# Kernel optimization log

Measured on AMD Instinct MI355X. Metric: run time of the kernel, lower is better.

Reference implementation:

```python
import jax, jax.numpy as jnp
import numpy as np

N = 50000      # nodes
E = 800000     # edges (before self loops)
NFEAT = 128
HEADS = 4
NCLASS = 32    # per-head out channels of each GATConv
NHID = HEADS * NCLASS  # 128, inter-layer width
NEG_SLOPE = 0.2


def setup_inputs() -> dict:
    key = jax.random.key(0)
    ks = jax.random.split(key, 10)
    x = jax.random.normal(ks[0], (N, NFEAT), dtype=jnp.float32)
    adj = jax.random.randint(ks[1], (2, E), 0, N, dtype=jnp.int32)

    def glorot(k, shape):
        fan = shape[0] + shape[-1]
        return jax.random.normal(k, shape, dtype=jnp.float32) * jnp.sqrt(2.0 / fan)

    # conv1: nfeat -> heads*nclass
    W1 = glorot(ks[2], (NFEAT, HEADS * NCLASS))
    att_src1 = glorot(ks[3], (HEADS, NCLASS))
    att_dst1 = glorot(ks[4], (HEADS, NCLASS))
    b1 = jnp.zeros((HEADS * NCLASS,), dtype=jnp.float32)
    # conv2: nhid -> heads*nclass
    W2 = glorot(ks[5], (NHID, HEADS * NCLASS))
    att_src2 = glorot(ks[6], (HEADS, NCLASS))
    att_dst2 = glorot(ks[7], (HEADS, NCLASS))
    b2 = jnp.zeros((HEADS * NCLASS,), dtype=jnp.float32)
    return {"x": x, "adj": adj,
            "W1": W1, "att_src1": att_src1, "att_dst1": att_dst1, "b1": b1,
            "W2": W2, "att_src2": att_src2, "att_dst2": att_dst2, "b2": b2}


def gat_conv(x, src, dst, n, W, att_src, att_dst, bias):
    """PyG GATConv (concat=True, inference): gather -> edge attention -> segment softmax -> scatter."""
    H, C = att_src.shape
    h = (x @ W).reshape(n, H, C)                    # [N,H,C]
    a_s = jnp.sum(h * att_src[None], axis=-1)       # [N,H]
    a_d = jnp.sum(h * att_dst[None], axis=-1)       # [N,H]
    e = jax.nn.leaky_relu(a_s[src] + a_d[dst], NEG_SLOPE)  # [E,H]
    # numerically-stable segment softmax over edges grouped by destination node
    m = jax.ops.segment_max(e, dst, num_segments=n)        # [N,H]
    m = jnp.where(jnp.isfinite(m), m, 0.0)
    ex = jnp.exp(e - m[dst])                               # [E,H]
    denom = jax.ops.segment_sum(ex, dst, num_segments=n)   # [N,H]
    alpha = ex / (denom[dst] + 1e-16)                      # [E,H]
    out = jax.ops.segment_sum(h[src] * alpha[:, :, None], dst, num_segments=n)  # [N,H,C]
    return out.reshape(n, H * C) + bias


def reference(x, adj, W1, att_src1, att_dst1, b1, W2, att_src2, att_dst2, b2):
    # PyG GATConv adds self loops by default
    loops = jnp.arange(N, dtype=adj.dtype)
    src = jnp.concatenate([adj[0], loops])
    dst = jnp.concatenate([adj[1], loops])
    h = jax.nn.relu(gat_conv(x, src, dst, N, W1, att_src1, att_dst1, b1))
    # dropout is identity in eval mode
    out = gat_conv(h, src, dst, N, W2, att_src2, att_dst2, b2)
    return out
```

## Files before the change

### kernel.cpp

```cpp
#include <hip/hip_runtime.h>
#include <hip/hip_fp16.h>

#define N_NODES 50000
#define E_EDGES 800000
#define ETOT    (E_EDGES + N_NODES)
#define NF      128
#define HEADS   4
#define NC      32
#define LOG2E   1.44269504088896340736f
#define ASTRIDE 136
#define CAP     96

#define NBUCK   196
#define EPB     4096
#define NBLKA   ((ETOT + EPB - 1) / EPB)
#define PARTN   (NBUCK * NBLKA)
#define NBLKS   ((PARTN + 255) / 256)
#define WCB     65

typedef __attribute__((ext_vector_type(8))) short short8v;
typedef __attribute__((ext_vector_type(4))) float f32x4;

__device__ inline ushort rne_bf16(float x) {
    uint u = __float_as_uint(x);
    return (ushort)((u + 0x7fff + ((u >> 16) & 1)) >> 16);
}
__device__ inline float h2f_lo(uint u) { return __half2float(__ushort_as_half((ushort)(u & 0xffffu))); }
__device__ inline float h2f_hi(uint u) { return __half2float(__ushort_as_half((ushort)(u >> 16))); }

__device__ inline void wconv_body(int wb, int tid, const float* __restrict__ W,
                                  const float* __restrict__ att_src,
                                  const float* __restrict__ att_dst,
                                  ushort* __restrict__ Wt) {
    if (wb < 64) {
        int i = wb * 256 + tid;
        int k = i >> 7, n = i & 127;
        Wt[n * 144 + k] = rne_bf16(W[i]);
    } else {
        for (int j = tid; j < 1024; j += 256) {
            int k = j >> 3, o = j & 7;
            int h = o & 3;
            const float* av = (o < 4) ? att_src : att_dst;
            float s = 0.f;
            #pragma unroll
            for (int c = 0; c < 32; ++c) s += W[k * 128 + h * 32 + c] * av[h * 32 + c];
            Wt[(128 + o) * 144 + k] = rne_bf16(s * LOG2E);
        }
        for (int j = tid; j < 8 * 144; j += 256)
            Wt[(136 + (j / 144)) * 144 + (j % 144)] = 0;
    }
}

__global__ __launch_bounds__(256) void prep_kernel(const int* __restrict__ adj,
                                                   int* __restrict__ partials,
                                                   const float* __restrict__ W1,
                                                   const float* __restrict__ as1,
                                                   const float* __restrict__ ad1,
                                                   ushort* __restrict__ Wt1,
                                                   const float* __restrict__ W2,
                                                   const float* __restrict__ as2,
                                                   const float* __restrict__ ad2,
                                                   ushort* __restrict__ Wt2) {
    __shared__ int lc[NBUCK];
    int b = blockIdx.x, tid = threadIdx.x;
    if (b < NBLKA) {
        for (int i = tid; i < NBUCK; i += 256) lc[i] = 0;
        __syncthreads();
        int base = b * EPB;
        #pragma unroll
        for (int i = 0; i < EPB / 256; ++i) {
            int e = base + i * 256 + tid;
            if (e < ETOT) {
                int dst = (e < E_EDGES) ? adj[E_EDGES + e] : (e - E_EDGES);
                atomicAdd(&lc[dst >> 8], 1);
            }
        }
        __syncthreads();
        for (int i = tid; i < NBUCK; i += 256) partials[i * NBLKA + b] = lc[i];
    } else {
        int wb = b - NBLKA;
        if (wb < WCB) wconv_body(wb, tid, W1, as1, ad1, Wt1);
        else          wconv_body(wb - WCB, tid, W2, as2, ad2, Wt2);
    }
}

__device__ inline int block_incl_scan(int v, int* sh4) {
    int lane = threadIdx.x & 63, wid = threadIdx.x >> 6;
    int s = v;
    #pragma unroll
    for (int ofs = 1; ofs < 64; ofs <<= 1) {
        int t = __shfl_up(s, ofs);
        if (lane >= ofs) s += t;
    }
    if (lane == 63) sh4[wid] = s;
    __syncthreads();
    int add = 0;
    #pragma unroll
    for (int k = 0; k < 3; ++k) if (k < wid) add += sh4[k];
    return s + add;
}

__global__ __launch_bounds__(256) void bsum2_kernel(const int* __restrict__ partials,
                                                    int* __restrict__ bsum) {
    __shared__ int sh4[4];
    int i = blockIdx.x * 256 + threadIdx.x;
    int v = (i < PARTN) ? partials[i] : 0;
    int s = block_incl_scan(v, sh4);
    if (threadIdx.x == 255) bsum[blockIdx.x] = s;
}

__global__ __launch_bounds__(256) void scan_bsums2_kernel(const int* __restrict__ bsum,
                                                          int* __restrict__ bofs) {
    __shared__ int sh4[4];
    int i = threadIdx.x;
    int v = (i < NBLKS) ? bsum[i] : 0;
    int s = block_incl_scan(v, sh4);
    if (i < NBLKS) bofs[i] = s - v;
}

__global__ __launch_bounds__(256) void scan_final2_kernel(const int* __restrict__ partials,
                                                          const int* __restrict__ bofs,
                                                          int* __restrict__ pscan) {
    __shared__ int sh4[4];
    int i = blockIdx.x * 256 + threadIdx.x;
    int v = (i < PARTN) ? partials[i] : 0;
    int s = block_incl_scan(v, sh4);
    if (i < PARTN) pscan[i] = bofs[blockIdx.x] + s - v;
}

__global__ __launch_bounds__(256) void pass_scatter_kernel(const int* __restrict__ adj,
                                                           const int* __restrict__ pscan,
                                                           int2* __restrict__ ebuf) {
    __shared__ int lc[NBUCK];
    int tid = threadIdx.x;
    for (int i = tid; i < NBUCK; i += 256) lc[i] = 0;
    __syncthreads();
    int base = blockIdx.x * EPB;
    #pragma unroll
    for (int i = 0; i < EPB / 256; ++i) {
        int e = base + i * 256 + tid;
        if (e < ETOT) {
            int src, dst;
            if (e < E_EDGES) { src = adj[e]; dst = adj[E_EDGES + e]; }
            else             { src = dst = e - E_EDGES; }
            int b = dst >> 8;
            int r = atomicAdd(&lc[b], 1);
            ebuf[pscan[b * NBLKA + blockIdx.x] + r] = make_int2(src, dst);
        }
    }
}

__global__ __launch_bounds__(256) void pass_build_kernel(const int2* __restrict__ ebuf,
                                                         const int* __restrict__ pscan,
                                                         int* __restrict__ cnt,
                                                         int* __restrict__ slots) {
    __shared__ int lc[256];
    int tid = threadIdx.x;
    int b = blockIdx.x;
    lc[tid] = 0;
    __syncthreads();
    int base = pscan[b * NBLKA];
    int end  = (b == NBUCK - 1) ? ETOT : pscan[(b + 1) * NBLKA];
    for (int e = base + tid; e < end; e += 256) {
        int2 sd = ebuf[e];
        int d = sd.y & 255;
        int r = atomicAdd(&lc[d], 1);
        slots[(size_t)sd.y * CAP + r] = sd.x;
    }
    __syncthreads();
    int dst = b * 256 + tid;
    if (dst < N_NODES) cnt[dst] = lc[tid];
}

template<bool BF16IN>
__global__ __launch_bounds__(256) void gemm_mfma_kernel(const void* __restrict__ Xv_,
                                                        const ushort* __restrict__ Wt,
                                                        ushort* __restrict__ Hf,
                                                        float* __restrict__ a_s,
                                                        float* __restrict__ a_d, int nrows) {
    __shared__ ushort Abf[64 * ASTRIDE];
    int tid = threadIdx.x;
    int r0 = blockIdx.x * 64;
    int rleft = nrows - r0;

    if (BF16IN) {
        const uint4* Xv = (const uint4*)((const ushort*)Xv_ + (size_t)r0 * NF);
        #pragma unroll
        for (int p = 0; p < 4; ++p) {
            int i = p * 256 + tid;
            int row = i >> 4, c8 = i & 15;
            uint4 v = (row < rleft) ? Xv[row * 16 + c8] : make_uint4(0u, 0u, 0u, 0u);
            *(uint4*)&Abf[row * ASTRIDE + c8 * 8] = v;
        }
    } else {
        const float4* Xv = (const float4*)((const float*)Xv_ + (size_t)r0 * NF);
        #pragma unroll
        for (int p = 0; p < 8; ++p) {
            int i = p * 256 + tid;
            int row = i >> 5, c4 = i & 31;
            float4 v = (row < rleft) ? Xv[row * 32 + c4] : make_float4(0.f, 0.f, 0.f, 0.f);
            ushort4 hv;
            hv.x = rne_bf16(v.x); hv.y = rne_bf16(v.y);
            hv.z = rne_bf16(v.z); hv.w = rne_bf16(v.w);
            *(ushort4*)&Abf[row * ASTRIDE + c4 * 4] = hv;
        }
    }
    __syncthreads();

    int wv = tid >> 6;
    int l = tid & 63;
    int lr = l & 15;
    int lk = l >> 4;
    int rowb = wv * 16;

    short8v a[4];
    #pragma unroll
    for (int kc = 0; kc < 4; ++kc)
        a[kc] = *(const short8v*)&Abf[(rowb + lr) * ASTRIDE + kc * 32 + lk * 8];

    f32x4 acc[9];
    #pragma unroll
    for (int ct = 0; ct < 9; ++ct) acc[ct] = (f32x4){0.f, 0.f, 0.f, 0.f};

    #pragma unroll
    for (int ct = 0; ct < 9; ++ct) {
        #pragma unroll
        for (int kc = 0; kc < 4; ++kc) {
            short8v b = *(const short8v*)&Wt[(ct * 16 + lr) * 144 + kc * 32 + lk * 8];
            acc[ct] = __builtin_amdgcn_mfma_f32_16x16x32_bf16(a[kc], b, acc[ct], 0, 0, 0);
        }
    }

    int rbase = r0 + rowb + lk * 4;
    #pragma unroll
    for (int ct = 0; ct < 8; ++ct) {
        int col = ct * 16 + lr;
        #pragma unroll
        for (int ri = 0; ri < 4; ++ri) {
            int r = rbase + ri;
            if (r < nrows) Hf[(size_t)r * NF + col] = __half_as_ushort(__float2half(acc[ct][ri]));
        }
    }
    if (lr < 8) {
        #pragma unroll
        for (int ri = 0; ri < 4; ++ri) {
            int r = rbase + ri;
            if (r < nrows) {
                if (lr < 4) a_s[(size_t)r * 4 + lr] = acc[8][ri];
                else        a_d[(size_t)r * 4 + (lr - 4)] = acc[8][ri];
            }
        }
    }
}

template<int WRITE_BF16>
__global__ __launch_bounds__(256) void agg_kernel(const ushort* __restrict__ Hf,
                                                  const float* __restrict__ a_s,
                                                  const float* __restrict__ a_d,
                                                  const int* __restrict__ cnt,
                                                  const int* __restrict__ slots,
                                                  const float* __restrict__ bias,
                                                  void* __restrict__ Out) {
    int lane = threadIdx.x & 63;
    int node = blockIdx.x * 4 + (threadIdx.x >> 6);
    if (node >= N_NODES) return;
    int q = lane >> 4;
    int t = lane & 15;
    int h = t >> 2;
    float adn = a_d[node * 4 + h];
    int deg = cnt[node];
    const int* row = slots + (size_t)node * CAP;
    const uint4* H4 = (const uint4*)Hf;
    float acc[8];
    #pragma unroll
    for (int k = 0; k < 8; ++k) acc[k] = 0.f;
    float denom = 0.f;

    for (int j = 0; j < deg; j += 8) {
        int sv[2]; float ev[2]; uint4 hv[2]; bool ok[2];
        #pragma unroll
        for (int u = 0; u < 2; ++u) {
            int idx = j + u * 4 + q;
            ok[u] = idx < deg;
            sv[u] = row[ok[u] ? idx : 0];
        }
        #pragma unroll
        for (int u = 0; u < 2; ++u) ev[u] = a_s[sv[u] * 4 + h];
        #pragma unroll
        for (int u = 0; u < 2; ++u) hv[u] = H4[(size_t)sv[u] * 16 + t];
        #pragma unroll
        for (int u = 0; u < 2; ++u) {
            float e = ev[u] + adn;
            e = (e > 0.f) ? e : 0.2f * e;
            float w = ok[u] ? exp2f(e) : 0.f;
            denom += w;
            acc[0] = fmaf(h2f_lo(hv[u].x), w, acc[0]);
            acc[1] = fmaf(h2f_hi(hv[u].x), w, acc[1]);
            acc[2] = fmaf(h2f_lo(hv[u].y), w, acc[2]);
            acc[3] = fmaf(h2f_hi(hv[u].y), w, acc[3]);
            acc[4] = fmaf(h2f_lo(hv[u].z), w, acc[4]);
            acc[5] = fmaf(h2f_hi(hv[u].z), w, acc[5]);
            acc[6] = fmaf(h2f_lo(hv[u].w), w, acc[6]);
            acc[7] = fmaf(h2f_hi(hv[u].w), w, acc[7]);
        }
    }
    #pragma unroll
    for (int ofs = 16; ofs < 64; ofs <<= 1) {
        denom += __shfl_xor(denom, ofs);
        #pragma unroll
        for (int k = 0; k < 8; ++k) acc[k] += __shfl_xor(acc[k], ofs);
    }
    if (q == 0) {
        float inv = 1.f / (denom + 1e-16f);
        float4 b0 = ((const float4*)bias)[t * 2];
        float4 b1 = ((const float4*)bias)[t * 2 + 1];
        float v0 = acc[0] * inv + b0.x, v1 = acc[1] * inv + b0.y;
        float v2 = acc[2] * inv + b0.z, v3 = acc[3] * inv + b0.w;
        float v4 = acc[4] * inv + b1.x, v5 = acc[5] * inv + b1.y;
        float v6 = acc[6] * inv + b1.z, v7 = acc[7] * inv + b1.w;
        if (WRITE_BF16) {
            v0 = fmaxf(v0, 0.f); v1 = fmaxf(v1, 0.f); v2 = fmaxf(v2, 0.f); v3 = fmaxf(v3, 0.f);
            v4 = fmaxf(v4, 0.f); v5 = fmaxf(v5, 0.f); v6 = fmaxf(v6, 0.f); v7 = fmaxf(v7, 0.f);
            uint4 pv;
            pv.x = (uint)rne_bf16(v0) | ((uint)rne_bf16(v1) << 16);
            pv.y = (uint)rne_bf16(v2) | ((uint)rne_bf16(v3) << 16);
            pv.z = (uint)rne_bf16(v4) | ((uint)rne_bf16(v5) << 16);
            pv.w = (uint)rne_bf16(v6) | ((uint)rne_bf16(v7) << 16);
            ((uint4*)((ushort*)Out + (size_t)node * NF))[t] = pv;
        } else {
            float4* orow = (float4*)((float*)Out + (size_t)node * NF);
            orow[t * 2]     = make_float4(v0, v1, v2, v3);
            orow[t * 2 + 1] = make_float4(v4, v5, v6, v7);
        }
    }
}

extern "C" void kernel_launch(void* const* d_in, const int* in_sizes, int n_in,
                              void* d_out, int out_size, void* d_ws, size_t ws_size,
                              hipStream_t stream) {
    const float* x        = (const float*)d_in[0];
    const int*   adj      = (const int*)  d_in[1];
    const float* W1       = (const float*)d_in[2];
    const float* att_src1 = (const float*)d_in[3];
    const float* att_dst1 = (const float*)d_in[4];
    const float* b1       = (const float*)d_in[5];
    const float* W2       = (const float*)d_in[6];
    const float* att_src2 = (const float*)d_in[7];
    const float* att_dst2 = (const float*)d_in[8];
    const float* b2       = (const float*)d_in[9];
    float* out = (float*)d_out;

    float* a_s  = (float*)d_ws;
    float* a_d  = a_s + (size_t)N_NODES * HEADS;
    ushort* Hf  = (ushort*)(a_d + (size_t)N_NODES * HEADS);
    ushort* obf = Hf + (size_t)N_NODES * NF;
    ushort* Wt1 = obf + (size_t)N_NODES * NF;
    ushort* Wt2 = Wt1 + 144 * 144;
    int* cnt     = (int*)(Wt2 + 144 * 144);
    int* slots   = cnt + N_NODES;
    int* partials= slots + (size_t)N_NODES * CAP;
    int* pscan   = partials + PARTN;
    int* bsum    = pscan + PARTN;
    int* bofs    = bsum + NBLKS;
    int2* ebuf   = (int2*)(bofs + NBLKS + 2);

    prep_kernel<<<NBLKA + 2 * WCB, 256, 0, stream>>>(adj, partials,
                                                     W1, att_src1, att_dst1, Wt1,
                                                     W2, att_src2, att_dst2, Wt2);
    bsum2_kernel<<<NBLKS, 256, 0, stream>>>(partials, bsum);
    scan_bsums2_kernel<<<1, 256, 0, stream>>>(bsum, bofs);
    scan_final2_kernel<<<NBLKS, 256, 0, stream>>>(partials, bofs, pscan);
    pass_scatter_kernel<<<NBLKA, 256, 0, stream>>>(adj, pscan, ebuf);
    pass_build_kernel<<<NBUCK, 256, 0, stream>>>(ebuf, pscan, cnt, slots);

    gemm_mfma_kernel<false><<<(N_NODES + 63) / 64, 256, 0, stream>>>(x, Wt1, Hf, a_s, a_d, N_NODES);
    agg_kernel<1><<<(N_NODES + 3) / 4, 256, 0, stream>>>(Hf, a_s, a_d, cnt, slots, b1, obf);

    gemm_mfma_kernel<true><<<(N_NODES + 63) / 64, 256, 0, stream>>>(obf, Wt2, Hf, a_s, a_d, N_NODES);
    agg_kernel<0><<<(N_NODES + 3) / 4, 256, 0, stream>>>(Hf, a_s, a_d, cnt, slots, b2, out);
}
```

Before: 149.3 us.

## Fuse CSR build pipeline into one cooperative kernel with grid syncs

Merges the six preprocessing kernels (bucket count plus weight conversion, three scan stages, scatter and slot build) into one cooperative launch that separates phases with grid-wide barriers. The aim is to remove five kernel launch gaps and their inter-kernel idle time. In exchange, every phase runs with the same grid size, roughly 338 blocks, so most blocks sit idle in the small scan phases. It also depends on all blocks being co-resident and on the cost of each grid.sync.

Measured after the change: 352.0 us. 136% more time.

```diff
diff --git a/kernel.cpp b/kernel.cpp
--- a/kernel.cpp
+++ b/kernel.cpp
@@ -1,5 +1,8 @@
 #include <hip/hip_runtime.h>
 #include <hip/hip_fp16.h>
+#include <hip/hip_cooperative_groups.h>
+
+namespace cg = cooperative_groups;
 
 #define N_NODES 50000
 #define E_EDGES 800000
@@ -17,6 +20,7 @@
 #define PARTN   (NBUCK * NBLKA)
 #define NBLKS   ((PARTN + 255) / 256)
 #define WCB     65
+#define COOPB   (NBLKA + 2 * WCB)
 
 typedef __attribute__((ext_vector_type(8))) short short8v;
 typedef __attribute__((ext_vector_type(4))) float f32x4;
@@ -51,18 +55,43 @@
     }
 }
 
-__global__ __launch_bounds__(256) void prep_kernel(const int* __restrict__ adj,
-                                                   int* __restrict__ partials,
-                                                   const float* __restrict__ W1,
-                                                   const float* __restrict__ as1,
-                                                   const float* __restrict__ ad1,
-                                                   ushort* __restrict__ Wt1,
-                                                   const float* __restrict__ W2,
-                                                   const float* __restrict__ as2,
-                                                   const float* __restrict__ ad2,
-                                                   ushort* __restrict__ Wt2) {
-    __shared__ int lc[NBUCK];
+__device__ inline int block_incl_scan(int v, int* sh4) {
+    int lane = threadIdx.x & 63, wid = threadIdx.x >> 6;
+    int s = v;
+    #pragma unroll
+    for (int ofs = 1; ofs < 64; ofs <<= 1) {
+        int t = __shfl_up(s, ofs);
+        if (lane >= ofs) s += t;
+    }
+    if (lane == 63) sh4[wid] = s;
+    __syncthreads();
+    int add = 0;
+    #pragma unroll
+    for (int k = 0; k < 3; ++k) if (k < wid) add += sh4[k];
+    return s + add;
+}
+
+__global__ __launch_bounds__(256) void csr_coop_kernel(const int* __restrict__ adj,
+                                                       int* __restrict__ partials,
+                                                       const float* __restrict__ W1,
+                                                       const float* __restrict__ as1,
+                                                       const float* __restrict__ ad1,
+                                                       ushort* __restrict__ Wt1,
+                                                       const float* __restrict__ W2,
+                                                       const float* __restrict__ as2,
+                                                       const float* __restrict__ ad2,
+                                                       ushort* __restrict__ Wt2,
+                                                       int* __restrict__ bsum,
+                                                       int* __restrict__ bofs,
+                                                       int* __restrict__ pscan,
+                                                       int2* __restrict__ ebuf,
+                                                       int* __restrict__ cnt,
+                                                       int* __restrict__ slots) {
+    cg::grid_group grid = cg::this_grid();
+    __shared__ int lc[256];
+    __shared__ int sh4[4];
     int b = blockIdx.x, tid = threadIdx.x;
+
     if (b < NBLKA) {
         for (int i = tid; i < NBUCK; i += 256) lc[i] = 0;
         __syncthreads();
@@ -82,94 +111,65 @@
         if (wb < WCB) wconv_body(wb, tid, W1, as1, ad1, Wt1);
         else          wconv_body(wb - WCB, tid, W2, as2, ad2, Wt2);
     }
-}
-
-__device__ inline int block_incl_scan(int v, int* sh4) {
-    int lane = threadIdx.x & 63, wid = threadIdx.x >> 6;
-    int s = v;
-    #pragma unroll
-    for (int ofs = 1; ofs < 64; ofs <<= 1) {
-        int t = __shfl_up(s, ofs);
-        if (lane >= ofs) s += t;
-    }
-    if (lane == 63) sh4[wid] = s;
-    __syncthreads();
-    int add = 0;
-    #pragma unroll
-    for (int k = 0; k < 3; ++k) if (k < wid) add += sh4[k];
-    return s + add;
-}
-
-__global__ __launch_bounds__(256) void bsum2_kernel(const int* __restrict__ partials,
-                                                    int* __restrict__ bsum) {
-    __shared__ int sh4[4];
-    int i = blockIdx.x * 256 + threadIdx.x;
-    int v = (i < PARTN) ? partials[i] : 0;
-    int s = block_incl_scan(v, sh4);
-    if (threadIdx.x == 255) bsum[blockIdx.x] = s;
-}
-
-__global__ __launch_bounds__(256) void scan_bsums2_kernel(const int* __restrict__ bsum,
-                                                          int* __restrict__ bofs) {
-    __shared__ int sh4[4];
-    int i = threadIdx.x;
-    int v = (i < NBLKS) ? bsum[i] : 0;
-    int s = block_incl_scan(v, sh4);
-    if (i < NBLKS) bofs[i] = s - v;
-}
-
-__global__ __launch_bounds__(256) void scan_final2_kernel(const int* __restrict__ partials,
-                                                          const int* __restrict__ bofs,
-                                                          int* __restrict__ pscan) {
-    __shared__ int sh4[4];
-    int i = blockIdx.x * 256 + threadIdx.x;
-    int v = (i < PARTN) ? partials[i] : 0;
-    int s = block_incl_scan(v, sh4);
-    if (i < PARTN) pscan[i] = bofs[blockIdx.x] + s - v;
-}
-
-__global__ __launch_bounds__(256) void pass_scatter_kernel(const int* __restrict__ adj,
-                                                           const int* __restrict__ pscan,
-                                                           int2* __restrict__ ebuf) {
-    __shared__ int lc[NBUCK];
-    int tid = threadIdx.x;
-    for (int i = tid; i < NBUCK; i += 256) lc[i] = 0;
-    __syncthreads();
-    int base = blockIdx.x * EPB;
-    #pragma unroll
-    for (int i = 0; i < EPB / 256; ++i) {
-        int e = base + i * 256 + tid;
-        if (e < ETOT) {
-            int src, dst;
-            if (e < E_EDGES) { src = adj[e]; dst = adj[E_EDGES + e]; }
-            else             { src = dst = e - E_EDGES; }
-            int b = dst >> 8;
-            int r = atomicAdd(&lc[b], 1);
-            ebuf[pscan[b * NBLKA + blockIdx.x] + r] = make_int2(src, dst);
-        }
-    }
-}
-
-__global__ __launch_bounds__(256) void pass_build_kernel(const int2* __restrict__ ebuf,
-                                                         const int* __restrict__ pscan,
-                                                         int* __restrict__ cnt,
-                                                         int* __restrict__ slots) {
-    __shared__ int lc[256];
-    int tid = threadIdx.x;
-    int b = blockIdx.x;
-    lc[tid] = 0;
-    __syncthreads();
-    int base = pscan[b * NBLKA];
-    int end  = (b == NBUCK - 1) ? ETOT : pscan[(b + 1) * NBLKA];
-    for (int e = base + tid; e < end; e += 256) {
-        int2 sd = ebuf[e];
-        int d = sd.y & 255;
-        int r = atomicAdd(&lc[d], 1);
-        slots[(size_t)sd.y * CAP + r] = sd.x;
-    }
-    __syncthreads();
-    int dst = b * 256 + tid;
-    if (dst < N_NODES) cnt[dst] = lc[tid];
+    grid.sync();
+
+    if (b < NBLKS) {
+        int i = b * 256 + tid;
+        int v = (i < PARTN) ? partials[i] : 0;
+        int s = block_incl_scan(v, sh4);
+        if (tid == 255) bsum[b] = s;
+    }
+    grid.sync();
+
+    if (b == 0) {
+        int v = (tid < NBLKS) ? bsum[tid] : 0;
+        int s = block_incl_scan(v, sh4);
+        if (tid < NBLKS) bofs[tid] = s - v;
+    }
+    grid.sync();
+
+    if (b < NBLKS) {
+        int i = b * 256 + tid;
+        int v = (i < PARTN) ? partials[i] : 0;
+        int s = block_incl_scan(v, sh4);
+        if (i < PARTN) pscan[i] = bofs[b] + s - v;
+    }
+    grid.sync();
+
+    if (b < NBLKA) {
+        for (int i = tid; i < NBUCK; i += 256) lc[i] = 0;
+        __syncthreads();
+        int base = b * EPB;
+        #pragma unroll
+        for (int i = 0; i < EPB / 256; ++i) {
+            int e = base + i * 256 + tid;
+            if (e < ETOT) {
+                int src, dst;
+                if (e < E_EDGES) { src = adj[e]; dst = adj[E_EDGES + e]; }
+                else             { src = dst = e - E_EDGES; }
+                int bk = dst >> 8;
+                int r = atomicAdd(&lc[bk], 1);
+                ebuf[pscan[bk * NBLKA + b] + r] = make_int2(src, dst);
+            }
+        }
+    }
+    grid.sync();
+
+    if (b < NBUCK) {
+        lc[tid] = 0;
+        __syncthreads();
+        int base = pscan[b * NBLKA];
+        int end  = (b == NBUCK - 1) ? ETOT : pscan[(b + 1) * NBLKA];
+        for (int e = base + tid; e < end; e += 256) {
+            int2 sd = ebuf[e];
+            int d = sd.y & 255;
+            int r = atomicAdd(&lc[d], 1);
+            slots[(size_t)sd.y * CAP + r] = sd.x;
+        }
+        __syncthreads();
+        int dst = b * 256 + tid;
+        if (dst < N_NODES) cnt[dst] = lc[tid];
+    }
 }
 
 template<bool BF16IN>
@@ -364,14 +364,15 @@
     int* bofs    = bsum + NBLKS;
     int2* ebuf   = (int2*)(bofs + NBLKS + 2);
 
-    prep_kernel<<<NBLKA + 2 * WCB, 256, 0, stream>>>(adj, partials,
-                                                     W1, att_src1, att_dst1, Wt1,
-                                                     W2, att_src2, att_dst2, Wt2);
-    bsum2_kernel<<<NBLKS, 256, 0, stream>>>(partials, bsum);
-    scan_bsums2_kernel<<<1, 256, 0, stream>>>(bsum, bofs);
-    scan_final2_kernel<<<NBLKS, 256, 0, stream>>>(partials, bofs, pscan);
-    pass_scatter_kernel<<<NBLKA, 256, 0, stream>>>(adj, pscan, ebuf);
-    pass_build_kernel<<<NBUCK, 256, 0, stream>>>(ebuf, pscan, cnt, slots);
+    {
+        void* args[] = {(void*)&adj, (void*)&partials,
+                        (void*)&W1, (void*)&att_src1, (void*)&att_dst1, (void*)&Wt1,
+                        (void*)&W2, (void*)&att_src2, (void*)&att_dst2, (void*)&Wt2,
+                        (void*)&bsum, (void*)&bofs, (void*)&pscan,
+                        (void*)&ebuf, (void*)&cnt, (void*)&slots};
+        hipLaunchCooperativeKernel((const void*)csr_coop_kernel, dim3(COOPB), dim3(256),
+                                   args, 0, stream);
+    }
 
     gemm_mfma_kernel<false><<<(N_NODES + 63) / 64, 256, 0, stream>>>(x, Wt1, Hf, a_s, a_d, N_NODES);
     agg_kernel<1><<<(N_NODES + 3) / 4, 256, 0, stream>>>(Hf, a_s, a_d, cnt, slots, b1, obf);
```

## Merge block-sum scan into final scan and co-launch edge scatter with layer-1 GEMM

Applied to the files above, without the earlier changes.

Removes the single-block scan_bsums kernel: each scan_final block now recomputes its own prefix offset from the block sums. The edge-scatter pass and the layer-1 GEMM, which do not depend on each other, are merged into one heterogeneous kernel whose blocks branch on blockIdx, so both run concurrently. This cuts two launches and their serialization gaps. In exchange each scan block does redundant work, and the merged kernel has to size its shared memory for the larger of the two roles.

Result: faster. 140.5 us, median of 2 (-5.8%).

```diff
diff --git a/kernel.cpp b/kernel.cpp
--- a/kernel.cpp
+++ b/kernel.cpp
@@ -109,45 +109,137 @@
     if (threadIdx.x == 255) bsum[blockIdx.x] = s;
 }
 
-__global__ __launch_bounds__(256) void scan_bsums2_kernel(const int* __restrict__ bsum,
-                                                          int* __restrict__ bofs) {
-    __shared__ int sh4[4];
-    int i = threadIdx.x;
-    int v = (i < NBLKS) ? bsum[i] : 0;
-    int s = block_incl_scan(v, sh4);
-    if (i < NBLKS) bofs[i] = s - v;
-}
-
 __global__ __launch_bounds__(256) void scan_final2_kernel(const int* __restrict__ partials,
-                                                          const int* __restrict__ bofs,
+                                                          const int* __restrict__ bsum,
                                                           int* __restrict__ pscan) {
     __shared__ int sh4[4];
-    int i = blockIdx.x * 256 + threadIdx.x;
+    __shared__ int bofs_sh;
+    int b = blockIdx.x, tid = threadIdx.x;
+    int pv = (tid < NBLKS && tid < b) ? bsum[tid] : 0;
+    int ps = block_incl_scan(pv, sh4);
+    if (tid == 255) bofs_sh = ps;
+    __syncthreads();
+    int i = b * 256 + tid;
     int v = (i < PARTN) ? partials[i] : 0;
     int s = block_incl_scan(v, sh4);
-    if (i < PARTN) pscan[i] = bofs[blockIdx.x] + s - v;
-}
-
-__global__ __launch_bounds__(256) void pass_scatter_kernel(const int* __restrict__ adj,
-                                                           const int* __restrict__ pscan,
-                                                           int2* __restrict__ ebuf) {
-    __shared__ int lc[NBUCK];
-    int tid = threadIdx.x;
-    for (int i = tid; i < NBUCK; i += 256) lc[i] = 0;
-    __syncthreads();
-    int base = blockIdx.x * EPB;
-    #pragma unroll
-    for (int i = 0; i < EPB / 256; ++i) {
-        int e = base + i * 256 + tid;
-        if (e < ETOT) {
-            int src, dst;
-            if (e < E_EDGES) { src = adj[e]; dst = adj[E_EDGES + e]; }
-            else             { src = dst = e - E_EDGES; }
-            int b = dst >> 8;
-            int r = atomicAdd(&lc[b], 1);
-            ebuf[pscan[b * NBLKA + blockIdx.x] + r] = make_int2(src, dst);
-        }
-    }
+    if (i < PARTN) pscan[i] = bofs_sh + s - v;
+}
+
+template<bool BF16IN>
+__device__ inline void gemm_body(ushort* __restrict__ Abf, int tid, int r0,
+                                 const void* __restrict__ Xv_, const ushort* __restrict__ Wt,
+                                 ushort* __restrict__ Hf, float* __restrict__ a_s,
+                                 float* __restrict__ a_d, int nrows) {
+    int rleft = nrows - r0;
+    if (BF16IN) {
+        const uint4* Xv = (const uint4*)((const ushort*)Xv_ + (size_t)r0 * NF);
+        #pragma unroll
+        for (int p = 0; p < 4; ++p) {
+            int i = p * 256 + tid;
+            int row = i >> 4, c8 = i & 15;
+            uint4 v = (row < rleft) ? Xv[row * 16 + c8] : make_uint4(0u, 0u, 0u, 0u);
+            *(uint4*)&Abf[row * ASTRIDE + c8 * 8] = v;
+        }
+    } else {
+        const float4* Xv = (const float4*)((const float*)Xv_ + (size_t)r0 * NF);
+        #pragma unroll
+        for (int p = 0; p < 8; ++p) {
+            int i = p * 256 + tid;
+            int row = i >> 5, c4 = i & 31;
+            float4 v = (row < rleft) ? Xv[row * 32 + c4] : make_float4(0.f, 0.f, 0.f, 0.f);
+            ushort4 hv;
+            hv.x = rne_bf16(v.x); hv.y = rne_bf16(v.y);
+            hv.z = rne_bf16(v.z); hv.w = rne_bf16(v.w);
+            *(ushort4*)&Abf[row * ASTRIDE + c4 * 4] = hv;
+        }
+    }
+    __syncthreads();
+
+    int wv = tid >> 6;
+    int l = tid & 63;
+    int lr = l & 15;
+    int lk = l >> 4;
+    int rowb = wv * 16;
+
+    short8v a[4];
+    #pragma unroll
+    for (int kc = 0; kc < 4; ++kc)
+        a[kc] = *(const short8v*)&Abf[(rowb + lr) * ASTRIDE + kc * 32 + lk * 8];
+
+    f32x4 acc[9];
+    #pragma unroll
+    for (int ct = 0; ct < 9; ++ct) acc[ct] = (f32x4){0.f, 0.f, 0.f, 0.f};
+
+    #pragma unroll
+    for (int ct = 0; ct < 9; ++ct) {
+        #pragma unroll
+        for (int kc = 0; kc < 4; ++kc) {
+            short8v b = *(const short8v*)&Wt[(ct * 16 + lr) * 144 + kc * 32 + lk * 8];
+            acc[ct] = __builtin_amdgcn_mfma_f32_16x16x32_bf16(a[kc], b, acc[ct], 0, 0, 0);
+        }
+    }
+
+    int rbase = r0 + rowb + lk * 4;
+    #pragma unroll
+    for (int ct = 0; ct < 8; ++ct) {
+        int col = ct * 16 + lr;
+        #pragma unroll
+        for (int ri = 0; ri < 4; ++ri) {
+            int r = rbase + ri;
+            if (r < nrows) Hf[(size_t)r * NF + col] = __half_as_ushort(__float2half(acc[ct][ri]));
+        }
+    }
+    if (lr < 8) {
+        #pragma unroll
+        for (int ri = 0; ri < 4; ++ri) {
+            int r = rbase + ri;
+            if (r < nrows) {
+                if (lr < 4) a_s[(size_t)r * 4 + lr] = acc[8][ri];
+                else        a_d[(size_t)r * 4 + (lr - 4)] = acc[8][ri];
+            }
+        }
+    }
+}
+
+__global__ __launch_bounds__(256) void mid_kernel(const int* __restrict__ adj,
+                                                  const int* __restrict__ pscan,
+                                                  int2* __restrict__ ebuf,
+                                                  const float* __restrict__ X,
+                                                  const ushort* __restrict__ Wt,
+                                                  ushort* __restrict__ Hf,
+                                                  float* __restrict__ a_s,
+                                                  float* __restrict__ a_d, int nrows) {
+    __shared__ ushort Abf[64 * ASTRIDE];
+    int b = blockIdx.x, tid = threadIdx.x;
+    if (b < NBLKA) {
+        int* lc = (int*)Abf;
+        for (int i = tid; i < NBUCK; i += 256) lc[i] = 0;
+        __syncthreads();
+        int base = b * EPB;
+        #pragma unroll
+        for (int i = 0; i < EPB / 256; ++i) {
+            int e = base + i * 256 + tid;
+            if (e < ETOT) {
+                int src, dst;
+                if (e < E_EDGES) { src = adj[e]; dst = adj[E_EDGES + e]; }
+                else             { src = dst = e - E_EDGES; }
+                int bk = dst >> 8;
+                int r = atomicAdd(&lc[bk], 1);
+                ebuf[pscan[bk * NBLKA + b] + r] = make_int2(src, dst);
+            }
+        }
+    } else {
+        gemm_body<false>(Abf, tid, (b - NBLKA) * 64, X, Wt, Hf, a_s, a_d, nrows);
+    }
+}
+
+__global__ __launch_bounds__(256) void gemm_mfma_kernel(const void* __restrict__ Xv_,
+                                                        const ushort* __restrict__ Wt,
+                                                        ushort* __restrict__ Hf,
+                                                        float* __restrict__ a_s,
+                                                        float* __restrict__ a_d, int nrows) {
+    __shared__ ushort Abf[64 * ASTRIDE];
+    gemm_body<true>(Abf, threadIdx.x, blockIdx.x * 64, Xv_, Wt, Hf, a_s, a_d, nrows);
 }
 
 __global__ __launch_bounds__(256) void pass_build_kernel(const int2* __restrict__ ebuf,
@@ -170,87 +262,6 @@
     __syncthreads();
     int dst = b * 256 + tid;
     if (dst < N_NODES) cnt[dst] = lc[tid];
-}
-
-template<bool BF16IN>
-__global__ __launch_bounds__(256) void gemm_mfma_kernel(const void* __restrict__ Xv_,
-                                                        const ushort* __restrict__ Wt,
-                                                        ushort* __restrict__ Hf,
-                                                        float* __restrict__ a_s,
-                                                        float* __restrict__ a_d, int nrows) {
-    __shared__ ushort Abf[64 * ASTRIDE];
-    int tid = threadIdx.x;
-    int r0 = blockIdx.x * 64;
-    int rleft = nrows - r0;
-
-    if (BF16IN) {
-        const uint4* Xv = (const uint4*)((const ushort*)Xv_ + (size_t)r0 * NF);
-        #pragma unroll
-        for (int p = 0; p < 4; ++p) {
-            int i = p * 256 + tid;
-            int row = i >> 4, c8 = i & 15;
-            uint4 v = (row < rleft) ? Xv[row * 16 + c8] : make_uint4(0u, 0u, 0u, 0u);
-            *(uint4*)&Abf[row * ASTRIDE + c8 * 8] = v;
-        }
-    } else {
-        const float4* Xv = (const float4*)((const float*)Xv_ + (size_t)r0 * NF);
-        #pragma unroll
-        for (int p = 0; p < 8; ++p) {
-            int i = p * 256 + tid;
-            int row = i >> 5, c4 = i & 31;
-            float4 v = (row < rleft) ? Xv[row * 32 + c4] : make_float4(0.f, 0.f, 0.f, 0.f);
-            ushort4 hv;
-            hv.x = rne_bf16(v.x); hv.y = rne_bf16(v.y);
-            hv.z = rne_bf16(v.z); hv.w = rne_bf16(v.w);
-            *(ushort4*)&Abf[row * ASTRIDE + c4 * 4] = hv;
-        }
-    }
-    __syncthreads();
-
-    int wv = tid >> 6;
-    int l = tid & 63;
-    int lr = l & 15;
-    int lk = l >> 4;
-    int rowb = wv * 16;
-
-    short8v a[4];
-    #pragma unroll
-    for (int kc = 0; kc < 4; ++kc)
-        a[kc] = *(const short8v*)&Abf[(rowb + lr) * ASTRIDE + kc * 32 + lk * 8];
-
-    f32x4 acc[9];
-    #pragma unroll
-    for (int ct = 0; ct < 9; ++ct) acc[ct] = (f32x4){0.f, 0.f, 0.f, 0.f};
-
-    #pragma unroll
-    for (int ct = 0; ct < 9; ++ct) {
-        #pragma unroll
-        for (int kc = 0; kc < 4; ++kc) {
-            short8v b = *(const short8v*)&Wt[(ct * 16 + lr) * 144 + kc * 32 + lk * 8];
-            acc[ct] = __builtin_amdgcn_mfma_f32_16x16x32_bf16(a[kc], b, acc[ct], 0, 0, 0);
-        }
-    }
-
-    int rbase = r0 + rowb + lk * 4;
-    #pragma unroll
-    for (int ct = 0; ct < 8; ++ct) {
-        int col = ct * 16 + lr;
-        #pragma unroll
-        for (int ri = 0; ri < 4; ++ri) {
-            int r = rbase + ri;
-            if (r < nrows) Hf[(size_t)r * NF + col] = __half_as_ushort(__float2half(acc[ct][ri]));
-        }
-    }
-    if (lr < 8) {
-        #pragma unroll
-        for (int ri = 0; ri < 4; ++ri) {
-            int r = rbase + ri;
-            if (r < nrows) {
-                if (lr < 4) a_s[(size_t)r * 4 + lr] = acc[8][ri];
-                else        a_d[(size_t)r * 4 + (lr - 4)] = acc[8][ri];
-            }
-        }
-    }
 }
 
 template<int WRITE_BF16>
@@ -361,21 +372,17 @@
     int* partials= slots + (size_t)N_NODES * CAP;
     int* pscan   = partials + PARTN;
     int* bsum    = pscan + PARTN;
-    int* bofs    = bsum + NBLKS;
-    int2* ebuf   = (int2*)(bofs + NBLKS + 2);
+    int2* ebuf   = (int2*)(bsum + NBLKS + 3);
 
     prep_kernel<<<NBLKA + 2 * WCB, 256, 0, stream>>>(adj, partials,
                                                      W1, att_src1, att_dst1, Wt1,
                                                      W2, att_src2, att_dst2, Wt2);
     bsum2_kernel<<<NBLKS, 256, 0, stream>>>(partials, bsum);
-    scan_bsums2_kernel<<<1, 256, 0, stream>>>(bsum, bofs);
-    scan_final2_kernel<<<NBLKS, 256, 0, stream>>>(partials, bofs, pscan);
-    pass_scatter_kernel<<<NBLKA, 256, 0, stream>>>(adj, pscan, ebuf);
+    scan_final2_kernel<<<NBLKS, 256, 0, stream>>>(partials, bsum, pscan);
+    mid_kernel<<<NBLKA + (N_NODES + 63) / 64, 256, 0, stream>>>(adj, pscan, ebuf,
+                                                                x, Wt1, Hf, a_s, a_d, N_NODES);
     pass_build_kernel<<<NBUCK, 256, 0, stream>>>(ebuf, pscan, cnt, slots);
-
-    gemm_mfma_kernel<false><<<(N_NODES + 63) / 64, 256, 0, stream>>>(x, Wt1, Hf, a_s, a_d, N_NODES);
     agg_kernel<1><<<(N_NODES + 3) / 4, 256, 0, stream>>>(Hf, a_s, a_d, cnt, slots, b1, obf);
-
-    gemm_mfma_kernel<true><<<(N_NODES + 63) / 64, 256, 0, stream>>>(obf, Wt2, Hf, a_s, a_d, N_NODES);
+    gemm_mfma_kernel<<<(N_NODES + 63) / 64, 256, 0, stream>>>(obf, Wt2, Hf, a_s, a_d, N_NODES);
     agg_kernel<0><<<(N_NODES + 3) / 4, 256, 0, stream>>>(Hf, a_s, a_d, cnt, slots, b2, out);
 }
```
